# Performance work log

Measured on AMD Instinct MI355X. Metric: run time of the kernel, lower is better.

The kernel has to match this reference:

```python
import jax, jax.numpy as jnp
import numpy as np

K = 5
BN_EPS = 1e-5


def _knn(xyz1, xyz2, embedding_lens):
    # squared pairwise distances [B, N, S]
    d2 = (jnp.sum(xyz1 ** 2, -1)[:, :, None]
          + jnp.sum(xyz2 ** 2, -1)[:, None, :]
          - 2.0 * jnp.einsum('bnc,bsc->bns', xyz1, xyz2))
    S = xyz2.shape[1]
    valid2 = jnp.arange(S)[None, :] < embedding_lens[:, None]  # [B, S]
    d2 = jnp.where(valid2[:, None, :], d2, jnp.float32(1e10))
    neg, idx = jax.lax.top_k(-d2, K)  # K smallest distances
    return -neg, idx  # squared dists [B,N,K], indices [B,N,K]


def _masked_bn(x, mask_f, gamma, beta):
    # x: [B, N, C]; mask_f: [B, N, 1] float; stats over valid positions only
    cnt = jnp.sum(mask_f)
    mean = jnp.sum(x * mask_f, axis=(0, 1)) / cnt
    var = jnp.sum(((x - mean) ** 2) * mask_f, axis=(0, 1)) / cnt
    return (x - mean) * jax.lax.rsqrt(var + BN_EPS) * gamma + beta


def setup_inputs() -> dict:
    key = jax.random.key(0)
    ks = jax.random.split(key, 8)
    B, N, S, D1, D2 = 16, 2048, 512, 384, 384
    xyz1 = jax.random.normal(ks[0], (B, N, 3), jnp.float32)
    xyz2 = jax.random.normal(ks[1], (B, S, 3), jnp.float32)
    points1 = jax.random.normal(ks[2], (B, N, D1), jnp.float32)
    points2 = jax.random.normal(ks[3], (B, S, D2), jnp.float32)
    point_lens = jax.random.randint(ks[4], (B,), N // 2, N + 1).astype(jnp.int32)
    embedding_lens = jax.random.randint(ks[5], (B,), S // 2, S + 1).astype(jnp.int32)
    point_mask = jnp.arange(N)[None, :] < point_lens[:, None]  # [B, N] bool
    Cin = D1 + D2
    W0 = jax.random.normal(ks[6], (768, Cin), jnp.float32) * (1.0 / np.sqrt(Cin))
    W1 = jax.random.normal(ks[7], (384, 768), jnp.float32) * (1.0 / np.sqrt(768))
    return dict(xyz1=xyz1, xyz2=xyz2, points1=points1, points2=points2,
                point_lens=point_lens, embedding_lens=embedding_lens,
                point_mask=point_mask,
                W0=W0, g0=jnp.ones((768,), jnp.float32), b0=jnp.zeros((768,), jnp.float32),
                W1=W1, g1=jnp.ones((384,), jnp.float32), b1=jnp.zeros((384,), jnp.float32))


def reference(xyz1, xyz2, points1, points2, point_lens, embedding_lens,
              point_mask, W0, g0, b0, W1, g1, b1):
    B, N, _ = xyz1.shape
    D2 = points2.shape[-1]
    dists, idx = _knn(xyz1[..., :3], xyz2, embedding_lens)
    eps = jnp.finfo(dists.dtype).eps
    dist_recip = 1.0 / (dists + eps)                    # [B, N, K]
    weight = dist_recip / jnp.sum(dist_recip, axis=2, keepdims=True)
    # masked gather: points2[b, idx[b,n,k], :] -> [B, N, K, D2]
    gathered = jnp.take_along_axis(points2, idx.reshape(B, N * K)[..., None],
                                   axis=1).reshape(B, N, K, D2)
    interp = jnp.sum(gathered * weight[..., None], axis=2)  # [B, N, D2]
    x = jnp.concatenate([points1, interp], axis=-1)          # [B, N, D1+D2]
    mask_f = point_mask.astype(x.dtype)[..., None]           # [B, N, 1]
    for W, g, b in ((W0, g0, b0), (W1, g1, b1)):
        x = jnp.einsum('bnc,dc->bnd', x, W)  # 1x1 conv, no bias
        x = jax.nn.relu(_masked_bn(x, mask_f, g, b))
    return x
```

## Files before the change

### kernel.cpp

```cpp
#include <hip/hip_runtime.h>
#include <cstdint>
#include <cstddef>

typedef unsigned short u16;
typedef __bf16 bf16x8 __attribute__((ext_vector_type(8)));
typedef float    f32x4 __attribute__((ext_vector_type(4)));
typedef unsigned int u32x4 __attribute__((ext_vector_type(4)));

constexpr int BB   = 16;
constexpr int NN   = 2048;
constexpr int SS   = 512;
constexpr int DD   = 384;
constexpr int CIN  = 768;
constexpr int HID  = 768;
constexpr int OUTC = 384;
constexpr int MROWS = BB * NN;
constexpr float KNN_EPS = 1.1920929e-07f;
constexpr float BN_EPS  = 1e-5f;

constexpr size_t OFF_W0B  = 0;
constexpr size_t OFF_W1B  = OFF_W0B  + (size_t)HID*CIN*2;
constexpr size_t OFF_IDX  = OFF_W1B  + (size_t)OUTC*HID*2;
constexpr size_t OFF_WGT  = OFF_IDX  + (size_t)MROWS*5*4;
constexpr size_t OFF_SUM1 = OFF_WGT  + (size_t)MROWS*5*4;
constexpr size_t OFF_SUM2 = OFF_SUM1 + (size_t)HID*2*4;
constexpr size_t OFF_COEF1= OFF_SUM2 + (size_t)OUTC*2*4;
constexpr size_t OFF_COEF2= OFF_COEF1+ (size_t)HID*2*4;
constexpr size_t OFF_XCAT = OFF_COEF2+ (size_t)OUTC*2*4;
constexpr size_t OFF_H1   = OFF_XCAT + (size_t)MROWS*CIN*2;

__device__ inline float bf2f(u16 u){ unsigned int i = ((unsigned int)u)<<16; float f; __builtin_memcpy(&f,&i,4); return f; }
__device__ inline u16 f2bf(float f){ unsigned int x; __builtin_memcpy(&x,&f,4);
  unsigned int r = (x + 0x7fffu + ((x>>16)&1u)) >> 16; return (u16)r; }

__device__ inline void async16(const void* g, void* l){
  __builtin_amdgcn_global_load_lds((const __attribute__((address_space(1))) void*)g,
                                   (__attribute__((address_space(3))) void*)l, 16, 0, 0);
}

__global__ void cvtw_kernel(const float* __restrict__ W0, const float* __restrict__ W1,
                            u16* __restrict__ W0b, u16* __restrict__ W1b){
  int t = blockIdx.x*256 + threadIdx.x;
  if (t < HID*CIN)  W0b[t] = f2bf(W0[t]);
  if (t < OUTC*HID) W1b[t] = f2bf(W1[t]);
}

__global__ __launch_bounds__(256) void knn_kernel(const float* __restrict__ xyz1,
                                                  const float* __restrict__ xyz2,
                                                  const int* __restrict__ elens,
                                                  int* __restrict__ idxO, float* __restrict__ wO){
  __shared__ f32x4 sp[SS];
  const int tid = threadIdx.x;
  const int wv = tid >> 6, lane = tid & 63;
  const int wg = blockIdx.x*4 + wv;
  const int b = wg >> 11;
  const int n = wg & (NN-1);
  for (int s = tid; s < SS; s += 256){
    float x = xyz2[((size_t)b*SS + s)*3 + 0];
    float y = xyz2[((size_t)b*SS + s)*3 + 1];
    float z = xyz2[((size_t)b*SS + s)*3 + 2];
    f32x4 v; v[0]=x; v[1]=y; v[2]=z; v[3]=x*x+y*y+z*z;
    sp[s]=v;
  }
  __syncthreads();
  const size_t qoff = ((size_t)b*NN + n)*3;
  const float qx = xyz1[qoff+0], qy = xyz1[qoff+1], qz = xyz1[qoff+2];
  const float qq = qx*qx + qy*qy + qz*qz;
  const int Sl = elens[b];

  float d0=1e30f,d1=1e30f,d2v=1e30f,d3=1e30f,d4=1e30f;
  int   i0=0,i1=0,i2=0,i3=0,i4=0;
  #pragma unroll
  for (int j=0;j<8;j++){
    const int s = lane + j*64;
    f32x4 v = sp[s];
    float d = (s < Sl) ? (qq + v[3] - 2.f*(qx*v[0] + qy*v[1] + qz*v[2])) : 1e30f;
    bool lt4=d<d4, lt3=d<d3, lt2=d<d2v, lt1=d<d1, lt0=d<d0;
    float nd4 = lt3 ? d3 : (lt4 ? d : d4); int ni4 = lt3 ? i3 : (lt4 ? s : i4);
    float nd3 = lt2 ? d2v: (lt3 ? d : d3); int ni3 = lt2 ? i2 : (lt3 ? s : i3);
    float nd2 = lt1 ? d1 : (lt2 ? d : d2v);int ni2 = lt1 ? i1 : (lt2 ? s : i2);
    float nd1 = lt0 ? d0 : (lt1 ? d : d1); int ni1 = lt0 ? i0 : (lt1 ? s : i1);
    float nd0 = lt0 ? d  : d0;             int ni0 = lt0 ? s  : i0;
    d4=nd4;i4=ni4; d3=nd3;i3=ni3; d2v=nd2;i2=ni2; d1=nd1;i1=ni1; d0=nd0;i0=ni0;
  }
  float outd[5]; int outi[5];
  #pragma unroll
  for (int r=0;r<5;r++){
    float bd = d0; int bs = i0;
    #pragma unroll
    for (int m=1;m<64;m<<=1){
      float od = __shfl_xor(bd, m, 64);
      int   os = __shfl_xor(bs, m, 64);
      if (od < bd || (od == bd && os < bs)){ bd = od; bs = os; }
    }
    outd[r]=bd; outi[r]=bs;
    if (d0 == bd && i0 == bs){ d0=d1;i0=i1; d1=d2v;i1=i2; d2v=d3;i2=i3; d3=d4;i3=i4; d4=1e30f;i4=0; }
  }
  if (lane == 0){
    float r0=1.f/(outd[0]+KNN_EPS), r1=1.f/(outd[1]+KNN_EPS), r2=1.f/(outd[2]+KNN_EPS),
          r3=1.f/(outd[3]+KNN_EPS), r4=1.f/(outd[4]+KNN_EPS);
    float inv = 1.f/(r0+r1+r2+r3+r4);
    size_t base = (size_t)wg*5;
    idxO[base+0]=outi[0]; idxO[base+1]=outi[1]; idxO[base+2]=outi[2]; idxO[base+3]=outi[3]; idxO[base+4]=outi[4];
    wO[base+0]=r0*inv; wO[base+1]=r1*inv; wO[base+2]=r2*inv; wO[base+3]=r3*inv; wO[base+4]=r4*inv;
  }
}

__global__ __launch_bounds__(384) void xcat_kernel(const float* __restrict__ p1,
                                                   const float* __restrict__ p2,
                                                   const int* __restrict__ idx,
                                                   const float* __restrict__ wgt,
                                                   u16* __restrict__ xcat){
  const int c = threadIdx.x;
  const int rowbase = blockIdx.x*8;
  for (int i=0;i<8;i++){
    const int row = rowbase + i;
    const int b = row >> 11;
    float v1 = p1[(size_t)row*DD + c];
    xcat[(size_t)row*CIN + c] = f2bf(v1);
    float acc = 0.f;
    size_t ib = (size_t)row*5;
    #pragma unroll
    for (int k=0;k<5;k++){
      int id = idx[ib+k]; float w = wgt[ib+k];
      acc += w * p2[((size_t)b*SS + id)*DD + c];
    }
    xcat[(size_t)row*CIN + DD + c] = f2bf(acc);
  }
}

template<bool OUT_BF16, bool FUSE_A, int GX, int K>
__global__ __launch_bounds__(256) void gemm_kernel(const u16* __restrict__ A,
                                                   const u16* __restrict__ Bw,
                                                   void* __restrict__ Cout,
                                                   const int* __restrict__ plen,
                                                   float* __restrict__ sums,
                                                   const float* __restrict__ cf){
  constexpr int NC = GX*128;
  constexpr int NSTEP = K/32;
  constexpr int NWG = GX*256;
  constexpr int CPX = NWG/8;
  __shared__ u16 As[2][128*32];
  __shared__ u16 Bs[2][128*32];
  const int tid  = threadIdx.x;
  const int lane = tid & 63, wv = tid >> 6;
  const int wr = wv >> 1, wc = wv & 1;
  const int l15 = lane & 15, l16 = lane >> 4;

  const int logical = (blockIdx.x & 7)*CPX + (blockIdx.x >> 3);
  const int bn = logical % GX, bm = logical / GX;

  int rowS[2], c8S[2];
  const u16* Ab[2]; const u16* Bb[2];
  #pragma unroll
  for (int j=0;j<2;j++){
    int ch = j*256 + wv*64 + lane;
    rowS[j] = ch >> 2; c8S[j] = ch & 3;
    Ab[j] = A  + (size_t)(bm*128 + rowS[j])*K + c8S[j]*8;
    Bb[j] = Bw + (size_t)(bn*128 + rowS[j])*K + c8S[j]*8;
  }

  auto stageA = [&](int nb, int kt){
    #pragma unroll
    for (int j=0;j<2;j++)
      async16(Ab[j] + kt*32, (char*)&As[nb][0] + (j*256 + wv*64)*16);
  };
  auto stageB = [&](int nb, int kt){
    #pragma unroll
    for (int j=0;j<2;j++)
      async16(Bb[j] + kt*32, (char*)&Bs[nb][0] + (j*256 + wv*64)*16);
  };
  u32x4 hv[2];
  auto loadA = [&](int kt){
    #pragma unroll
    for (int j=0;j<2;j++)
      hv[j] = *reinterpret_cast<const u32x4*>(Ab[j] + kt*32);
  };
  auto bnwrite = [&](int nb, int kt){
    #pragma unroll
    for (int j=0;j<2;j++){
      const int k0 = kt*32 + c8S[j]*8;
      float av[8], bv[8];
      *reinterpret_cast<f32x4*>(av)   = *reinterpret_cast<const f32x4*>(cf + k0);
      *reinterpret_cast<f32x4*>(av+4) = *reinterpret_cast<const f32x4*>(cf + k0 + 4);
      *reinterpret_cast<f32x4*>(bv)   = *reinterpret_cast<const f32x4*>(cf + K + k0);
      *reinterpret_cast<f32x4*>(bv+4) = *reinterpret_cast<const f32x4*>(cf + K + k0 + 4);
      u32x4 v = hv[j]; u32x4 o;
      #pragma unroll
      for (int q=0;q<4;q++){
        float lo = bf2f((u16)(v[q] & 0xffffu));
        float hi = bf2f((u16)(v[q] >> 16));
        lo = fmaxf(lo*av[2*q]   + bv[2*q],   0.f);
        hi = fmaxf(hi*av[2*q+1] + bv[2*q+1], 0.f);
        o[q] = (unsigned int)f2bf(lo) | ((unsigned int)f2bf(hi) << 16);
      }
      *reinterpret_cast<u32x4*>((char*)&As[nb][0] + (j*256 + wv*64)*16 + lane*16) = o;
    }
  };

  f32x4 acc[4][4] = {};

  if constexpr (FUSE_A) loadA(0); else stageA(0, 0);
  stageB(0, 0);
  if constexpr (FUSE_A) bnwrite(0, 0);
  __syncthreads();

  int cur = 0;
  for (int kt=0; kt<NSTEP; ++kt){
    const bool pf = (kt+1 < NSTEP);
    if (pf){
      if constexpr (FUSE_A) loadA(kt+1); else stageA(cur^1, kt+1);
      stageB(cur^1, kt+1);
    }
    bf16x8 af[4], bfr[4];
    #pragma unroll
    for (int m=0;m<4;m++){
      int r = wr*64 + m*16 + l15;
      af[m] = *reinterpret_cast<const bf16x8*>(&As[cur][r*32 + l16*8]);
    }
    #pragma unroll
    for (int n=0;n<4;n++){
      int c = wc*64 + n*16 + l15;
      bfr[n] = *reinterpret_cast<const bf16x8*>(&Bs[cur][c*32 + l16*8]);
    }
    #pragma unroll
    for (int m=0;m<4;m++)
      #pragma unroll
      for (int n=0;n<4;n++)
        acc[m][n] = __builtin_amdgcn_mfma_f32_16x16x32_bf16(af[m], bfr[n], acc[m][n], 0, 0, 0);
    if constexpr (FUSE_A) { if (pf) bnwrite(cur^1, kt+1); }
    __syncthreads();
    cur ^= 1;
  }

  #pragma unroll
  for (int m=0;m<4;m++){
    int r0 = bm*128 + wr*64 + m*16 + l16*4;
    #pragma unroll
    for (int n=0;n<4;n++){
      int c = bn*128 + wc*64 + n*16 + l15;
      #pragma unroll
      for (int r=0;r<4;r++){
        size_t off = (size_t)(r0+r)*NC + c;
        if (OUT_BF16) ((u16*)Cout)[off] = f2bf(acc[m][n][r]);
        else          ((float*)Cout)[off] = acc[m][n][r];
      }
    }
  }

  const int pl = plen[bm >> 4];
  const int rbase = (bm & 15)*128 + wr*64 + l16*4;
  float cs[4] = {0.f,0.f,0.f,0.f}, cs2[4] = {0.f,0.f,0.f,0.f};
  #pragma unroll
  for (int m=0;m<4;m++){
    #pragma unroll
    for (int r=0;r<4;r++){
      if (rbase + m*16 + r < pl){
        #pragma unroll
        for (int n=0;n<4;n++){
          float v = acc[m][n][r];
          cs[n] += v; cs2[n] += v*v;
        }
      }
    }
  }
  #pragma unroll
  for (int n=0;n<4;n++){
    cs[n]  += __shfl_xor(cs[n], 16, 64);  cs[n]  += __shfl_xor(cs[n], 32, 64);
    cs2[n] += __shfl_xor(cs2[n], 16, 64); cs2[n] += __shfl_xor(cs2[n], 32, 64);
  }
  float* lsum = (float*)&As[0][0];
  lsum[tid] = 0.f;
  __syncthreads();
  if (l16 == 0){
    #pragma unroll
    for (int n=0;n<4;n++){
      int col = wc*64 + n*16 + l15;
      atomicAdd(&lsum[col], cs[n]);
      atomicAdd(&lsum[128 + col], cs2[n]);
    }
  }
  __syncthreads();
  if (tid < 128)       atomicAdd(&sums[bn*128 + tid], lsum[tid]);
  else                 atomicAdd(&sums[NC + bn*128 + (tid-128)], lsum[tid]);
}

__global__ void coef_kernel(const float* __restrict__ sums, const int* __restrict__ plen,
                            const float* __restrict__ g, const float* __restrict__ bta,
                            float* __restrict__ coef, int C){
  int c = threadIdx.x;
  if (c >= C) return;
  float cnt = 0.f;
  for (int b=0;b<BB;b++) cnt += (float)plen[b];
  float mean = sums[c] / cnt;
  float var  = sums[C + c] / cnt - mean*mean;
  var = fmaxf(var, 0.f);
  float a = g[c] * rsqrtf(var + BN_EPS);
  coef[c] = a;
  coef[C + c] = bta[c] - mean*a;
}

__global__ __launch_bounds__(256) void final_kernel(float* __restrict__ Y,
                                                    const float* __restrict__ coef){
  size_t t = (size_t)blockIdx.x*256 + threadIdx.x;
  size_t f = t*4;
  int c = (int)(f % (size_t)OUTC);
  f32x4 v = *reinterpret_cast<const f32x4*>(Y + f);
  #pragma unroll
  for (int j=0;j<4;j++)
    v[j] = fmaxf(v[j]*coef[c+j] + coef[OUTC+c+j], 0.f);
  *reinterpret_cast<f32x4*>(Y + f) = v;
}

extern "C" void kernel_launch(void* const* d_in, const int* in_sizes, int n_in,
                              void* d_out, int out_size, void* d_ws, size_t ws_size,
                              hipStream_t stream){
  (void)in_sizes; (void)n_in; (void)out_size; (void)ws_size;
  const float* xyz1 = (const float*)d_in[0];
  const float* xyz2 = (const float*)d_in[1];
  const float* p1   = (const float*)d_in[2];
  const float* p2   = (const float*)d_in[3];
  const int*   plen = (const int*)d_in[4];
  const int*   elen = (const int*)d_in[5];
  const float* W0   = (const float*)d_in[7];
  const float* g0   = (const float*)d_in[8];
  const float* b0   = (const float*)d_in[9];
  const float* W1   = (const float*)d_in[10];
  const float* g1   = (const float*)d_in[11];
  const float* b1   = (const float*)d_in[12];
  float* out = (float*)d_out;
  char*  ws  = (char*)d_ws;

  u16*   W0b  = (u16*)  (ws + OFF_W0B);
  u16*   W1b  = (u16*)  (ws + OFF_W1B);
  int*   idxb = (int*)  (ws + OFF_IDX);
  float* wgtb = (float*)(ws + OFF_WGT);
  float* sum1 = (float*)(ws + OFF_SUM1);
  float* sum2 = (float*)(ws + OFF_SUM2);
  float* coef1= (float*)(ws + OFF_COEF1);
  float* coef2= (float*)(ws + OFF_COEF2);
  u16*   xcat = (u16*)  (ws + OFF_XCAT);
  u16*   h1   = (u16*)  (ws + OFF_H1);

  hipMemsetAsync(ws + OFF_SUM1, 0, (size_t)(HID*2 + OUTC*2)*4, stream);

  cvtw_kernel<<<(HID*CIN + 255)/256, 256, 0, stream>>>(W0, W1, W0b, W1b);
  knn_kernel<<<MROWS/4, 256, 0, stream>>>(xyz1, xyz2, elen, idxb, wgtb);
  xcat_kernel<<<MROWS/8, 384, 0, stream>>>(p1, p2, idxb, wgtb, xcat);

  gemm_kernel<true, false, 6, CIN><<<6*256, 256, 0, stream>>>(xcat, W0b, h1, plen, sum1, nullptr);
  coef_kernel<<<1, HID, 0, stream>>>(sum1, plen, g0, b0, coef1, HID);

  gemm_kernel<false, true, 3, HID><<<3*256, 256, 0, stream>>>(h1, W1b, out, plen, sum2, coef1);
  coef_kernel<<<1, OUTC, 0, stream>>>(sum2, plen, g1, b1, coef2, OUTC);
  final_kernel<<<(size_t)MROWS*OUTC/4/256, 256, 0, stream>>>(out, coef2);
}
```

Baseline: 189.2 us.

## Triple-buffer GEMM LDS tiles with explicit waitcnt and XOR swizzle

Moves the GEMM main loop from double to triple buffering of the B tiles (and of the A tiles when A is not fused), issuing async global-to-LDS loads two steps ahead. The blanket __syncthreads is replaced by an s_waitcnt with a partial vmcnt followed by s_barrier, so loads still in flight for a later stage are not drained. It also XOR-swizzles the 16-byte chunk column on both the LDS write and read sides to reduce bank conflicts on the fragment reads. The cost is more LDS per block, which may lower occupancy, and hand-written vmcnt counts that must exactly match the number of outstanding loads.

Measured after the change: 193.4 us. 2.2% more time.

```diff
diff --git a/kernel.cpp b/kernel.cpp
--- a/kernel.cpp
+++ b/kernel.cpp
@@ -140,41 +140,43 @@
   constexpr int NSTEP = K/32;
   constexpr int NWG = GX*256;
   constexpr int CPX = NWG/8;
-  __shared__ u16 As[2][128*32];
-  __shared__ u16 Bs[2][128*32];
+  constexpr int NAB = FUSE_A ? 2 : 3;
+  __shared__ u16 As[NAB][128*32];
+  __shared__ u16 Bs[3][128*32];
   const int tid  = threadIdx.x;
   const int lane = tid & 63, wv = tid >> 6;
   const int wr = wv >> 1, wc = wv & 1;
   const int l15 = lane & 15, l16 = lane >> 4;
+  const int sw  = (l15 >> 1) & 3;
 
   const int logical = (blockIdx.x & 7)*CPX + (blockIdx.x >> 3);
   const int bn = logical % GX, bm = logical / GX;
 
-  int rowS[2], c8S[2];
+  int c8S[2], ldso[2];
   const u16* Ab[2]; const u16* Bb[2];
   #pragma unroll
   for (int j=0;j<2;j++){
     int ch = j*256 + wv*64 + lane;
-    rowS[j] = ch >> 2; c8S[j] = ch & 3;
-    Ab[j] = A  + (size_t)(bm*128 + rowS[j])*K + c8S[j]*8;
-    Bb[j] = Bw + (size_t)(bn*128 + rowS[j])*K + c8S[j]*8;
+    int row = ch >> 2;
+    int c8 = (ch & 3) ^ ((ch >> 3) & 3);
+    c8S[j] = c8;
+    ldso[j] = (j*256 + wv*64)*16;
+    Ab[j] = A  + (size_t)(bm*128 + row)*K + c8*8;
+    Bb[j] = Bw + (size_t)(bn*128 + row)*K + c8*8;
   }
 
   auto stageA = [&](int nb, int kt){
     #pragma unroll
-    for (int j=0;j<2;j++)
-      async16(Ab[j] + kt*32, (char*)&As[nb][0] + (j*256 + wv*64)*16);
+    for (int j=0;j<2;j++) async16(Ab[j] + kt*32, (char*)&As[nb][0] + ldso[j]);
   };
   auto stageB = [&](int nb, int kt){
     #pragma unroll
-    for (int j=0;j<2;j++)
-      async16(Bb[j] + kt*32, (char*)&Bs[nb][0] + (j*256 + wv*64)*16);
+    for (int j=0;j<2;j++) async16(Bb[j] + kt*32, (char*)&Bs[nb][0] + ldso[j]);
   };
-  u32x4 hv[2];
+  u32x4 hv0, hv1;
   auto loadA = [&](int kt){
-    #pragma unroll
-    for (int j=0;j<2;j++)
-      hv[j] = *reinterpret_cast<const u32x4*>(Ab[j] + kt*32);
+    hv0 = *reinterpret_cast<const u32x4*>(Ab[0] + kt*32);
+    hv1 = *reinterpret_cast<const u32x4*>(Ab[1] + kt*32);
   };
   auto bnwrite = [&](int nb, int kt){
     #pragma unroll
@@ -185,7 +187,7 @@
       *reinterpret_cast<f32x4*>(av+4) = *reinterpret_cast<const f32x4*>(cf + k0 + 4);
       *reinterpret_cast<f32x4*>(bv)   = *reinterpret_cast<const f32x4*>(cf + K + k0);
       *reinterpret_cast<f32x4*>(bv+4) = *reinterpret_cast<const f32x4*>(cf + K + k0 + 4);
-      u32x4 v = hv[j]; u32x4 o;
+      u32x4 v = j ? hv1 : hv0; u32x4 o;
       #pragma unroll
       for (int q=0;q<4;q++){
         float lo = bf2f((u16)(v[q] & 0xffffu));
@@ -194,43 +196,68 @@
         hi = fmaxf(hi*av[2*q+1] + bv[2*q+1], 0.f);
         o[q] = (unsigned int)f2bf(lo) | ((unsigned int)f2bf(hi) << 16);
       }
-      *reinterpret_cast<u32x4*>((char*)&As[nb][0] + (j*256 + wv*64)*16 + lane*16) = o;
+      *reinterpret_cast<u32x4*>((char*)&As[nb][0] + ldso[j] + lane*16) = o;
     }
   };
 
   f32x4 acc[4][4] = {};
 
-  if constexpr (FUSE_A) loadA(0); else stageA(0, 0);
-  stageB(0, 0);
-  if constexpr (FUSE_A) bnwrite(0, 0);
-  __syncthreads();
-
-  int cur = 0;
+  if constexpr (FUSE_A){
+    loadA(0);
+    __builtin_amdgcn_sched_barrier(0);
+    stageB(0, 0); stageB(1, 1);
+    bnwrite(0, 0);
+    asm volatile("s_waitcnt vmcnt(2) lgkmcnt(0)" ::: "memory");
+    __builtin_amdgcn_s_barrier();
+  } else {
+    stageA(0, 0); stageB(0, 0);
+    stageA(1, 1); stageB(1, 1);
+    asm volatile("s_waitcnt vmcnt(4) lgkmcnt(0)" ::: "memory");
+    __builtin_amdgcn_s_barrier();
+  }
+
+  int rb = 0, wb = 2;
   for (int kt=0; kt<NSTEP; ++kt){
-    const bool pf = (kt+1 < NSTEP);
-    if (pf){
-      if constexpr (FUSE_A) loadA(kt+1); else stageA(cur^1, kt+1);
-      stageB(cur^1, kt+1);
-    }
+    const bool pf1 = (kt+1 < NSTEP), pf2 = (kt+2 < NSTEP);
+    if constexpr (FUSE_A){
+      if (pf1) loadA(kt+1);
+      __builtin_amdgcn_sched_barrier(0);
+      if (pf2) stageB(wb, kt+2);
+    } else {
+      if (pf2){ stageA(wb, kt+2); stageB(wb, kt+2); }
+    }
+
     bf16x8 af[4], bfr[4];
+    const int aslot = FUSE_A ? (kt & 1) : rb;
     #pragma unroll
     for (int m=0;m<4;m++){
       int r = wr*64 + m*16 + l15;
-      af[m] = *reinterpret_cast<const bf16x8*>(&As[cur][r*32 + l16*8]);
+      af[m] = *reinterpret_cast<const bf16x8*>(&As[aslot][r*32 + ((l16 ^ sw) << 3)]);
     }
     #pragma unroll
     for (int n=0;n<4;n++){
       int c = wc*64 + n*16 + l15;
-      bfr[n] = *reinterpret_cast<const bf16x8*>(&Bs[cur][c*32 + l16*8]);
+      bfr[n] = *reinterpret_cast<const bf16x8*>(&Bs[rb][c*32 + ((l16 ^ sw) << 3)]);
     }
     #pragma unroll
     for (int m=0;m<4;m++)
       #pragma unroll
       for (int n=0;n<4;n++)
         acc[m][n] = __builtin_amdgcn_mfma_f32_16x16x32_bf16(af[m], bfr[n], acc[m][n], 0, 0, 0);
-    if constexpr (FUSE_A) { if (pf) bnwrite(cur^1, kt+1); }
-    __syncthreads();
-    cur ^= 1;
+
+    if constexpr (FUSE_A){ if (pf1) bnwrite((kt+1)&1, kt+1); }
+
+    if (pf1){
+      if (pf2){
+        if constexpr (FUSE_A) asm volatile("s_waitcnt vmcnt(2) lgkmcnt(0)" ::: "memory");
+        else                  asm volatile("s_waitcnt vmcnt(4) lgkmcnt(0)" ::: "memory");
+      } else {
+        asm volatile("s_waitcnt vmcnt(0) lgkmcnt(0)" ::: "memory");
+      }
+      __builtin_amdgcn_s_barrier();
+    }
+    rb = (rb==2) ? 0 : rb+1;
+    wb = (wb==2) ? 0 : wb+1;
   }
 
   #pragma unroll
```

## Specialize first GEMM with 256x128 tiles, triple-buffered A and swizzled LDS

Applied to the files above, without the earlier changes.

Splits the templated GEMM into a dedicated first-layer kernel that uses 512-thread workgroups with 256x128 output tiles, a triple-buffered A stage and a double-buffered B stage in LDS. It also applies an XOR swizzle to reduce LDS bank conflicts and raises wave priority around the MFMA block. The second GEMM keeps its original structure with the unused template branches removed. The larger tile and deeper prefetch aim to improve reuse and hide global-load latency, at the cost of more LDS and registers per workgroup and therefore lower occupancy.

After: 209.0 us. +10.5%, slower.

```diff
diff --git a/kernel.cpp b/kernel.cpp
--- a/kernel.cpp
+++ b/kernel.cpp
@@ -129,13 +129,141 @@
   }
 }
 
-template<bool OUT_BF16, bool FUSE_A, int GX, int K>
-__global__ __launch_bounds__(256) void gemm_kernel(const u16* __restrict__ A,
-                                                   const u16* __restrict__ Bw,
-                                                   void* __restrict__ Cout,
-                                                   const int* __restrict__ plen,
-                                                   float* __restrict__ sums,
-                                                   const float* __restrict__ cf){
+__global__ __launch_bounds__(512) void gemm1_kernel(const u16* __restrict__ A,
+                                                    const u16* __restrict__ Bw,
+                                                    u16* __restrict__ Cout,
+                                                    const int* __restrict__ plen,
+                                                    float* __restrict__ sums){
+  constexpr int K   = CIN;
+  constexpr int NC  = HID;
+  constexpr int GXX = NC/128;
+  constexpr int NT  = K/32;
+  constexpr int NWG = (MROWS/256)*GXX;
+  constexpr int CPX = NWG/8;
+  __shared__ u16 Ash[3][8192];
+  __shared__ u16 Bsh[2][4096];
+
+  const int tid  = threadIdx.x;
+  const int lane = tid & 63, wv = tid >> 6;
+  const int wr = wv >> 2, wc = wv & 3;
+  const int l15 = lane & 15, l16 = lane >> 4;
+  const int swz = (l15 >> 1) & 3;
+
+  const int logical = (blockIdx.x & 7)*CPX + (blockIdx.x >> 3);
+  const int bn = logical % GXX, bm = logical / GXX;
+
+  const int chA0 = tid,      rA0 = chA0 >> 2, kA0 = (chA0 & 3) ^ ((chA0 >> 3) & 3);
+  const int chA1 = 512+tid,  rA1 = chA1 >> 2, kA1 = (chA1 & 3) ^ ((chA1 >> 3) & 3);
+  const int chB  = tid,      rB  = chB  >> 2, kB  = (chB  & 3) ^ ((chB  >> 3) & 3);
+  const u16* gA0 = A  + (size_t)(bm*256 + rA0)*K + kA0*8;
+  const u16* gA1 = A  + (size_t)(bm*256 + rA1)*K + kA1*8;
+  const u16* gB  = Bw + (size_t)(bn*128 + rB )*K + kB*8;
+
+  auto stageA = [&](int tt, int ab){
+    async16(gA0 + tt*32, (char*)&Ash[ab][0] + wv*1024);
+    async16(gA1 + tt*32, (char*)&Ash[ab][0] + 8192 + wv*1024);
+  };
+  auto stageB = [&](int tt, int bb){
+    async16(gB + tt*32, (char*)&Bsh[bb][0] + wv*1024);
+  };
+
+  int aoff[8], boff[2];
+  #pragma unroll
+  for (int m=0;m<8;m++) aoff[m] = (wr*128 + m*16 + l15)*32 + ((l16 ^ swz) << 3);
+  #pragma unroll
+  for (int n=0;n<2;n++) boff[n] = (wc*32 + n*16 + l15)*32 + ((l16 ^ swz) << 3);
+
+  f32x4 acc[8][2] = {};
+
+  stageA(0, 0); stageB(0, 0); stageA(1, 1);
+  asm volatile("s_waitcnt vmcnt(2)" ::: "memory");
+  __builtin_amdgcn_s_barrier();
+
+  auto step = [&](int t, int ab, int bb, int bbn, int abn2){
+    if (t+1 < NT) stageB(t+1, bbn);
+    if (t+2 < NT) stageA(t+2, abn2);
+    bf16x8 af[8], bfr[2];
+    #pragma unroll
+    for (int n=0;n<2;n++) bfr[n] = *reinterpret_cast<const bf16x8*>(&Bsh[bb][boff[n]]);
+    #pragma unroll
+    for (int m=0;m<8;m++) af[m] = *reinterpret_cast<const bf16x8*>(&Ash[ab][aoff[m]]);
+    __builtin_amdgcn_s_setprio(1);
+    #pragma unroll
+    for (int m=0;m<8;m++)
+      #pragma unroll
+      for (int n=0;n<2;n++)
+        acc[m][n] = __builtin_amdgcn_mfma_f32_16x16x32_bf16(af[m], bfr[n], acc[m][n], 0, 0, 0);
+    __builtin_amdgcn_s_setprio(0);
+    asm volatile("s_waitcnt vmcnt(2)" ::: "memory");
+    __builtin_amdgcn_s_barrier();
+  };
+
+  for (int t0=0; t0<NT; t0+=6){
+    step(t0+0, 0, 0, 1, 2);
+    step(t0+1, 1, 1, 0, 0);
+    step(t0+2, 2, 0, 1, 1);
+    step(t0+3, 0, 1, 0, 2);
+    step(t0+4, 1, 0, 1, 0);
+    step(t0+5, 2, 1, 0, 1);
+  }
+
+  #pragma unroll
+  for (int m=0;m<8;m++){
+    int r0 = bm*256 + wr*128 + m*16 + l16*4;
+    #pragma unroll
+    for (int n=0;n<2;n++){
+      int c = bn*128 + wc*32 + n*16 + l15;
+      #pragma unroll
+      for (int r=0;r<4;r++)
+        Cout[(size_t)(r0+r)*NC + c] = f2bf(acc[m][n][r]);
+    }
+  }
+
+  const int pl = plen[bm >> 3];
+  const int rbase = (bm & 7)*256 + wr*128 + l16*4;
+  float cs[2] = {0.f,0.f}, cs2[2] = {0.f,0.f};
+  #pragma unroll
+  for (int m=0;m<8;m++){
+    #pragma unroll
+    for (int r=0;r<4;r++){
+      if (rbase + m*16 + r < pl){
+        #pragma unroll
+        for (int n=0;n<2;n++){
+          float v = acc[m][n][r];
+          cs[n] += v; cs2[n] += v*v;
+        }
+      }
+    }
+  }
+  #pragma unroll
+  for (int n=0;n<2;n++){
+    cs[n]  += __shfl_xor(cs[n], 16, 64);  cs[n]  += __shfl_xor(cs[n], 32, 64);
+    cs2[n] += __shfl_xor(cs2[n], 16, 64); cs2[n] += __shfl_xor(cs2[n], 32, 64);
+  }
+  float* lsum = (float*)&Ash[0][0];
+  if (tid < 256) lsum[tid] = 0.f;
+  __syncthreads();
+  if (l16 == 0){
+    #pragma unroll
+    for (int n=0;n<2;n++){
+      int col = wc*32 + n*16 + l15;
+      atomicAdd(&lsum[col], cs[n]);
+      atomicAdd(&lsum[128 + col], cs2[n]);
+    }
+  }
+  __syncthreads();
+  if (tid < 128)       atomicAdd(&sums[bn*128 + tid], lsum[tid]);
+  else if (tid < 256)  atomicAdd(&sums[NC + bn*128 + (tid-128)], lsum[tid]);
+}
+
+__global__ __launch_bounds__(256) void gemm2_kernel(const u16* __restrict__ A,
+                                                    const u16* __restrict__ Bw,
+                                                    float* __restrict__ Cout,
+                                                    const int* __restrict__ plen,
+                                                    float* __restrict__ sums,
+                                                    const float* __restrict__ cf){
+  constexpr int GX = 3;
+  constexpr int K  = HID;
   constexpr int NC = GX*128;
   constexpr int NSTEP = K/32;
   constexpr int NWG = GX*256;
@@ -160,11 +288,6 @@
     Bb[j] = Bw + (size_t)(bn*128 + rowS[j])*K + c8S[j]*8;
   }
 
-  auto stageA = [&](int nb, int kt){
-    #pragma unroll
-    for (int j=0;j<2;j++)
-      async16(Ab[j] + kt*32, (char*)&As[nb][0] + (j*256 + wv*64)*16);
-  };
   auto stageB = [&](int nb, int kt){
     #pragma unroll
     for (int j=0;j<2;j++)
@@ -200,16 +323,16 @@
 
   f32x4 acc[4][4] = {};
 
-  if constexpr (FUSE_A) loadA(0); else stageA(0, 0);
+  loadA(0);
   stageB(0, 0);
-  if constexpr (FUSE_A) bnwrite(0, 0);
+  bnwrite(0, 0);
   __syncthreads();
 
   int cur = 0;
   for (int kt=0; kt<NSTEP; ++kt){
     const bool pf = (kt+1 < NSTEP);
     if (pf){
-      if constexpr (FUSE_A) loadA(kt+1); else stageA(cur^1, kt+1);
+      loadA(kt+1);
       stageB(cur^1, kt+1);
     }
     bf16x8 af[4], bfr[4];
@@ -228,7 +351,7 @@
       #pragma unroll
       for (int n=0;n<4;n++)
         acc[m][n] = __builtin_amdgcn_mfma_f32_16x16x32_bf16(af[m], bfr[n], acc[m][n], 0, 0, 0);
-    if constexpr (FUSE_A) { if (pf) bnwrite(cur^1, kt+1); }
+    if (pf) bnwrite(cur^1, kt+1);
     __syncthreads();
     cur ^= 1;
   }
@@ -240,11 +363,8 @@
     for (int n=0;n<4;n++){
       int c = bn*128 + wc*64 + n*16 + l15;
       #pragma unroll
-      for (int r=0;r<4;r++){
-        size_t off = (size_t)(r0+r)*NC + c;
-        if (OUT_BF16) ((u16*)Cout)[off] = f2bf(acc[m][n][r]);
-        else          ((float*)Cout)[off] = acc[m][n][r];
-      }
+      for (int r=0;r<4;r++)
+        Cout[(size_t)(r0+r)*NC + c] = acc[m][n][r];
     }
   }
 
@@ -348,10 +468,10 @@
   knn_kernel<<<MROWS/4, 256, 0, stream>>>(xyz1, xyz2, elen, idxb, wgtb);
   xcat_kernel<<<MROWS/8, 384, 0, stream>>>(p1, p2, idxb, wgtb, xcat);
 
-  gemm_kernel<true, false, 6, CIN><<<6*256, 256, 0, stream>>>(xcat, W0b, h1, plen, sum1, nullptr);
+  gemm1_kernel<<<(MROWS/256)*(HID/128), 512, 0, stream>>>(xcat, W0b, h1, plen, sum1);
   coef_kernel<<<1, HID, 0, stream>>>(sum1, plen, g0, b0, coef1, HID);
 
-  gemm_kernel<false, true, 3, HID><<<3*256, 256, 0, stream>>>(h1, W1b, out, plen, sum2, coef1);
+  gemm2_kernel<<<3*256, 256, 0, stream>>>(h1, W1b, out, plen, sum2, coef1);
   coef_kernel<<<1, OUTC, 0, stream>>>(sum2, plen, g1, b1, coef2, OUTC);
   final_kernel<<<(size_t)MROWS*OUTC/4/256, 256, 0, stream>>>(out, coef2);
 }
```
